# Optimization experiments

Measured on AMD Instinct MI355X. Metric: run time of the kernel, lower is better.

## Reference

```python
import jax, jax.numpy as jnp
import numpy as np

B, N, HID, IN_NF, L = 32, 64, 128, 32, 4


def _w(k, shape):
    fan_in = shape[-2]
    return jax.random.normal(k, shape, jnp.float32) / np.sqrt(fan_in).astype(np.float32)


def setup_inputs() -> dict:
    key = jax.random.key(0)
    ks = jax.random.split(key, 12)
    n_nodes = B * N
    # fully connected edges within each graph, offset for flat batch layout
    r, c = np.meshgrid(np.arange(N), np.arange(N), indexing='ij')
    m = r != c
    r, c = r[m], c[m]                      # (N*(N-1),)
    offs = (np.arange(B) * N)[:, None]
    edge_row = jnp.asarray((r[None] + offs).reshape(-1), dtype=jnp.int32)
    edge_col = jnp.asarray((c[None] + offs).reshape(-1), dtype=jnp.int32)
    n_edges = edge_row.shape[0]            # 129024
    return {
        'h': jax.random.normal(ks[0], (n_nodes, IN_NF), jnp.float32),
        'x': jax.random.normal(ks[1], (n_nodes, 3), jnp.float32),
        'edge_row': edge_row,
        'edge_col': edge_col,
        'edge_attr': jax.random.normal(ks[2], (n_edges, HID), jnp.float32) * 0.1,
        'emb_w': _w(ks[3], (IN_NF, HID)), 'emb_b': jnp.zeros((HID,), jnp.float32),
        'edge_w1': _w(ks[4], (L, 3 * HID + 1, HID)), 'edge_b1': jnp.zeros((L, HID), jnp.float32),
        'edge_w2': _w(ks[5], (L, HID, HID)), 'edge_b2': jnp.zeros((L, HID), jnp.float32),
        'node_w1': _w(ks[6], (L, 2 * HID, HID)), 'node_b1': jnp.zeros((L, HID), jnp.float32),
        'node_w2': _w(ks[7], (L, HID, HID)), 'node_b2': jnp.zeros((L, HID), jnp.float32),
        'coord_w1': _w(ks[8], (L, HID, HID)), 'coord_b1': jnp.zeros((L, HID), jnp.float32),
        'coord_w2': jax.random.normal(ks[9], (L, HID, 1), jnp.float32) * 0.001,  # xavier gain=0.001, no bias
    }


def reference(h, x, edge_row, edge_col, edge_attr,
              emb_w, emb_b,
              edge_w1, edge_b1, edge_w2, edge_b2,
              node_w1, node_b1, node_w2, node_b2,
              coord_w1, coord_b1, coord_w2):
    n_nodes = h.shape[0]
    silu = jax.nn.silu
    # degree for 'mean' coordinate aggregation (segments guaranteed nonempty via clip)
    ones = jnp.ones((edge_row.shape[0], 1), h.dtype)
    deg = jnp.clip(jax.ops.segment_sum(ones, edge_row, num_segments=n_nodes), 1.0)
    h = h @ emb_w + emb_b  # embedding_in
    for i in range(L):
        diff = x[edge_row] - x[edge_col]                 # (E,3)
        radial = jnp.sum(diff * diff, axis=1, keepdims=True)  # (E,1)
        # edge model: MLP([h_i, h_j, radial, edge_attr])
        e_in = jnp.concatenate([h[edge_row], h[edge_col], radial, edge_attr], axis=1)
        m = silu(silu(e_in @ edge_w1[i] + edge_b1[i]) @ edge_w2[i] + edge_b2[i])  # (E,HID)
        # coord model: mean-aggregated weighted differences
        trans = diff * (silu(m @ coord_w1[i] + coord_b1[i]) @ coord_w2[i])
        x = x + jax.ops.segment_sum(trans, edge_row, num_segments=n_nodes) / deg
        # node model with residual
        agg = jax.ops.segment_sum(m, edge_row, num_segments=n_nodes)
        n_in = jnp.concatenate([h, agg], axis=1)
        h = h + (silu(n_in @ node_w1[i] + node_b1[i]) @ node_w2[i] + node_b2[i])
        edge_attr = m  # backbone re-feeds edge_feat as next layer's edge_attr
    return h  # (B*N, HID); node_mask is None -> raw node embeddings returned
```

## Files before the change

kernel.cpp:

```cpp
#include <hip/hip_runtime.h>
#include <cstdint>
#include <cstddef>

#define HID    128
#define K1     385
#define NLAYER 4
#define NNODES 2048
#define NEDGES 129024
#define DEG    63
#define EPB    64
#define EBLOCKS (NEDGES / EPB)
#define EA_STRIDE 256
#define NPB    16
#define NBLOCKS (NNODES / NPB)

#define EIN_STRIDE 512
#define MBASE   16384
#define REDBASE 32768
#define RADBASE 33280
#define HR1BASE 33536
#define CB1BASE 34560
#define CW2BASE 35072
#define ELDS    35584

typedef __attribute__((ext_vector_type(8))) short short8;
typedef __attribute__((ext_vector_type(4))) float f32x4;

__device__ __forceinline__ unsigned pkbf(float a, float b) {
    unsigned r;
    asm("v_cvt_pk_bf16_f32 %0, %1, %2" : "=v"(r) : "v"(a), "v"(b));
    return r;
}
__device__ __forceinline__ unsigned short f2bf(float a) {
    return (unsigned short)pkbf(a, a);
}
__device__ __forceinline__ float silu_f(float v) {
    return v * __builtin_amdgcn_rcpf(1.0f + __expf(-v));
}

__global__ __launch_bounds__(64) void pack_all_kernel(
    const float* __restrict__ eW1, const float* __restrict__ eW2,
    const float* __restrict__ cW1, const float* __restrict__ nW1,
    const float* __restrict__ nW2,
    unsigned short* __restrict__ w1p, unsigned short* __restrict__ w1a,
    unsigned short* __restrict__ w2p, unsigned short* __restrict__ cw1p,
    unsigned short* __restrict__ nw1p, unsigned short* __restrict__ nw2p)
{
    int b = blockIdx.x;
    const float* src; unsigned short* dst; int KK, ls, mode;
    if (b < 256)      { src = eW1; dst = w1p;  KK = 8; ls = K1 * HID;      mode = 1; }
    else if (b < 384) { src = eW1; dst = w1a;  KK = 4; ls = K1 * HID;      mode = 0; b -= 256; }
    else if (b < 512) { src = eW2; dst = w2p;  KK = 4; ls = HID * HID;     mode = 0; b -= 384; }
    else if (b < 640) { src = cW1; dst = cw1p; KK = 4; ls = HID * HID;     mode = 0; b -= 512; }
    else if (b < 896) { src = nW1; dst = nw1p; KK = 8; ls = 2 * HID * HID; mode = 0; b -= 640; }
    else              { src = nW2; dst = nw2p; KK = 4; ls = HID * HID;     mode = 0; b -= 896; }
    const int tn = b & 7; b >>= 3;
    const int kk = b % KK;
    const int layer = b / KK;
    const int lane = threadIdx.x, lq = lane >> 4, lr = lane & 15;
    const float* s = src + (size_t)layer * ls;
    unsigned short* d = dst + (size_t)layer * (KK * 8 * 64 * 8)
                            + ((size_t)(kk * 8 + tn) * 64 + lane) * 8;
#pragma unroll
    for (int j = 0; j < 8; ++j) {
        const int kd = kk * 32 + lq * 8 + j;
        const int ka = mode ? (128 + kd + (kd >= 128 ? 1 : 0)) : kd;
        d[j] = f2bf(s[(size_t)ka * HID + tn * 16 + lr]);
    }
}

__global__ __launch_bounds__(128) void embed_kernel(
    const float* __restrict__ h_in, const float* __restrict__ emb_w,
    const float* __restrict__ emb_b, const float* __restrict__ eW1,
    const float* __restrict__ eB1,
    float* __restrict__ h_ws, unsigned short* __restrict__ h_bf,
    float* __restrict__ hr1, float* __restrict__ agg,
    const float* __restrict__ x_in, float* __restrict__ x_a)
{
    const int n = blockIdx.x;
    const int o = threadIdx.x;
    __shared__ float hin[32];
    __shared__ float hrow[HID];
    if (o < 32) hin[o] = h_in[n * 32 + o];
    __syncthreads();
    float acc = emb_b[o];
#pragma unroll
    for (int k = 0; k < 32; ++k) acc += hin[k] * emb_w[k * HID + o];
    h_ws[n * HID + o] = acc;
    h_bf[n * HID + o] = f2bf(acc);
    hrow[o] = acc;
    agg[n * HID + o] = 0.0f;
    if (o < 3) x_a[n * 3 + o] = x_in[n * 3 + o];
    __syncthreads();
    float a2 = eB1[o];
    for (int k = 0; k < HID; ++k) a2 += hrow[k] * eW1[k * HID + o];
    hr1[n * HID + o] = a2;
}

__global__ __launch_bounds__(512, 6) void edge_mfma_kernel(
    const unsigned short* __restrict__ h_bf, const float* __restrict__ x,
    const float* __restrict__ ea_f32, unsigned short* __restrict__ ea,
    const int first_layer, const float* __restrict__ hr1,
    const short8* __restrict__ w1p, const float* __restrict__ w256,
    const short8* __restrict__ w2p, const float* __restrict__ b2,
    const short8* __restrict__ cw1p, const float* __restrict__ cb1, const float* __restrict__ cw2,
    float* __restrict__ c_out, float* __restrict__ agg)
{
    __shared__ __align__(16) char smem[ELDS];
    float* red    = (float*)(smem + REDBASE);
    float* radial = (float*)(smem + RADBASE);
    float* hr1s   = (float*)(smem + HR1BASE);
    float* cb1s   = (float*)(smem + CB1BASE);
    float* cw2s   = (float*)(smem + CW2BASE);
    const int t = threadIdx.x;
    const int w = t >> 6, lane = t & 63, lq = lane >> 4, lr = lane & 15;
    const int ebase = blockIdx.x * EPB;
    const int n0 = ebase / DEG;
    const int esplit = DEG * (n0 + 1) - ebase;

    {
        const int s = t & 15, g = t >> 4;
#pragma unroll
        for (int j = 0; j < 2; ++j) {
            const int r = g + j * 32;
            const int e = ebase + r;
            const int row = n0 + (r >= esplit ? 1 : 0);
            const int jj = e - row * DEG;
            const int rl = row & 63;
            const int col = (row & ~63) + jj + (jj >= rl ? 1 : 0);
            const int swz = (r & 7) << 4;
            *(uint4*)(smem + r * EIN_STRIDE + ((s * 16) ^ swz)) =
                *(const uint4*)(h_bf + (size_t)col * HID + s * 8);
            uint4 v;
            if (first_layer) {
                const float4* ef = (const float4*)(ea_f32 + (size_t)e * HID);
                const float4 f0 = ef[s * 2], f1 = ef[s * 2 + 1];
                v.x = pkbf(f0.x, f0.y);
                v.y = pkbf(f0.z, f0.w);
                v.z = pkbf(f1.x, f1.y);
                v.w = pkbf(f1.z, f1.w);
            } else {
                v = *(const uint4*)(ea + (size_t)e * EA_STRIDE + s * 8);
            }
            *(uint4*)(smem + r * EIN_STRIDE + (((s + 16) * 16) ^ swz)) = v;
            if (s == 0) {
                const float dx = x[row * 3 + 0] - x[col * 3 + 0];
                const float dy = x[row * 3 + 1] - x[col * 3 + 1];
                const float dz = x[row * 3 + 2] - x[col * 3 + 2];
                radial[r] = dx * dx + dy * dy + dz * dz;
            }
        }
        if (t < 128) { cb1s[t] = cb1[t]; cw2s[t] = cw2[t]; }
        else if (t < 384) {
            const int i2 = t - 128;
            hr1s[i2] = hr1[(size_t)(n0 + (i2 >> 7)) * HID + (i2 & 127)];
        }
    }
    __syncthreads();

    const int c0 = w * 16 + lr;

    f32x4 acc1[4] = {};
#pragma unroll
    for (int kk = 0; kk < 8; ++kk) {
        const short8 bf = w1p[(kk * 8 + w) * 64 + lane];
#pragma unroll
        for (int mt = 0; mt < 4; ++mt) {
            const int r = mt * 16 + lr;
            const short8 af = *(const short8*)(smem + r * EIN_STRIDE +
                                ((kk * 64 + lq * 16) ^ ((r & 7) << 4)));
            acc1[mt] = __builtin_amdgcn_mfma_f32_16x16x32_bf16(af, bf, acc1[mt], 0, 0, 0);
        }
    }
    __syncthreads();

    {
        const float ww = w256[c0];
        const float ha = hr1s[c0], hb = hr1s[128 + c0];
#pragma unroll
        for (int mt = 0; mt < 4; ++mt)
#pragma unroll
            for (int reg = 0; reg < 4; ++reg) {
                const int r = mt * 16 + lq * 4 + reg;
                const float v = silu_f(acc1[mt][reg] + radial[r] * ww +
                                       (r < esplit ? ha : hb));
                *(unsigned short*)(smem + r * 256 + ((c0 * 2) ^ ((r & 7) << 4))) = f2bf(v);
            }
    }
    __syncthreads();

    f32x4 acc2[4] = {};
#pragma unroll
    for (int kk = 0; kk < 4; ++kk) {
        const short8 bf = w2p[(kk * 8 + w) * 64 + lane];
#pragma unroll
        for (int mt = 0; mt < 4; ++mt) {
            const int r = mt * 16 + lr;
            const short8 af = *(const short8*)(smem + r * 256 +
                                ((kk * 64 + lq * 16) ^ ((r & 7) << 4)));
            acc2[mt] = __builtin_amdgcn_mfma_f32_16x16x32_bf16(af, bf, acc2[mt], 0, 0, 0);
        }
    }
    {
        const float bb = b2[c0];
        float s0 = 0.0f, s1 = 0.0f;
#pragma unroll
        for (int mt = 0; mt < 4; ++mt)
#pragma unroll
            for (int reg = 0; reg < 4; ++reg) {
                const int r = mt * 16 + lq * 4 + reg;
                const float v = silu_f(acc2[mt][reg] + bb);
                if (r < esplit) s0 += v; else s1 += v;
                *(unsigned short*)(smem + MBASE + r * 256 + ((c0 * 2) ^ ((r & 7) << 4))) = f2bf(v);
            }
        s0 += __shfl_xor(s0, 16); s0 += __shfl_xor(s0, 32);
        s1 += __shfl_xor(s1, 16); s1 += __shfl_xor(s1, 32);
        if (lane < 16) {
            atomicAdd(&agg[(size_t)n0 * HID + c0], s0);
            atomicAdd(&agg[(size_t)(n0 + 1) * HID + c0], s1);
        }
    }
    __syncthreads();

    const int etile = w & 3, jhalf = w >> 2;
    f32x4 acc3[4] = {};
    {
        const int erow = etile * 16 + lr;
        const int eswz = (erow & 7) << 4;
#pragma unroll
        for (int kb = 0; kb < 4; ++kb) {
            const short8 mf = *(const short8*)(smem + MBASE + erow * 256 +
                                ((kb * 64 + lq * 16) ^ eswz));
#pragma unroll
            for (int jt = 0; jt < 4; ++jt) {
                const short8 af = cw1p[(kb * 8 + jhalf * 4 + jt) * 64 + lane];
                acc3[jt] = __builtin_amdgcn_mfma_f32_16x16x32_bf16(af, mf, acc3[jt], 0, 0, 0);
            }
        }
    }
    {
        const int s = t & 15, g = t >> 4;
#pragma unroll
        for (int j = 0; j < 2; ++j) {
            const int r = g + j * 32;
            const uint4 v = *(const uint4*)(smem + MBASE + r * 256 +
                                            ((s * 16) ^ ((r & 7) << 4)));
            *(uint4*)(ea + (size_t)(ebase + r) * EA_STRIDE + s * 8) = v;
        }
    }
    {
        float p = 0.0f;
#pragma unroll
        for (int jt = 0; jt < 4; ++jt)
#pragma unroll
            for (int reg = 0; reg < 4; ++reg) {
                const int j2 = jhalf * 64 + jt * 16 + lq * 4 + reg;
                p += silu_f(acc3[jt][reg] + cb1s[j2]) * cw2s[j2];
            }
        p += __shfl_xor(p, 16);
        p += __shfl_xor(p, 32);
        if (lane < 16) red[jhalf * 64 + etile * 16 + lane] = p;
    }
    __syncthreads();
    if (t < 64) c_out[ebase + t] = red[t] + red[64 + t];
}

__global__ __launch_bounds__(512, 4) void node_mfma_kernel(
    float* __restrict__ h_ws, unsigned short* __restrict__ h_bf,
    float* __restrict__ agg,
    const short8* __restrict__ nw1p, const float* __restrict__ nb1,
    const short8* __restrict__ nw2p, const float* __restrict__ nb2,
    const short8* __restrict__ w1a_next, const float* __restrict__ b1_next,
    float* __restrict__ hr1,
    const float* __restrict__ x_in, float* __restrict__ x_out,
    const float* __restrict__ c_ws,
    float* __restrict__ out, const int write_out, const int do_coord)
{
    __shared__ __align__(16) char smem[16384];
    const int t = threadIdx.x;
    const int w = t >> 6, lane = t & 63, lq = lane >> 4, lr = lane & 15;
    const int nb = blockIdx.x * NPB;

    {
        const int s = t & 31, g = t >> 5;
        const int node = nb + g;
        const int swz = (g & 7) << 4;
        if (s < 16) {
            *(uint4*)(smem + g * 512 + ((s * 16) ^ swz)) =
                *(const uint4*)(h_bf + (size_t)node * HID + s * 8);
        } else {
            const int q = s - 16;
            float4* agg4 = (float4*)(agg + (size_t)node * HID);
            const float4 a0 = agg4[q * 2], a1 = agg4[q * 2 + 1];
            agg4[q * 2]     = float4{0, 0, 0, 0};
            agg4[q * 2 + 1] = float4{0, 0, 0, 0};
            uint4 v;
            v.x = pkbf(a0.x, a0.y);
            v.y = pkbf(a0.z, a0.w);
            v.z = pkbf(a1.x, a1.y);
            v.w = pkbf(a1.z, a1.w);
            *(uint4*)(smem + g * 512 + ((s * 16) ^ swz)) = v;
        }
    }
    __syncthreads();

    const int c0 = w * 16 + lr;

    f32x4 acc1 = {};
#pragma unroll
    for (int kk = 0; kk < 8; ++kk) {
        const short8 bf = nw1p[(kk * 8 + w) * 64 + lane];
        const short8 af = *(const short8*)(smem + lr * 512 +
                            ((kk * 64 + lq * 16) ^ ((lr & 7) << 4)));
        acc1 = __builtin_amdgcn_mfma_f32_16x16x32_bf16(af, bf, acc1, 0, 0, 0);
    }
    __syncthreads();
    {
        const float bb = nb1[c0];
#pragma unroll
        for (int reg = 0; reg < 4; ++reg) {
            const int r = lq * 4 + reg;
            const float v = silu_f(acc1[reg] + bb);
            *(unsigned short*)(smem + 8192 + r * 256 + ((c0 * 2) ^ ((r & 7) << 4))) = f2bf(v);
        }
    }
    __syncthreads();
    f32x4 acc2 = {};
#pragma unroll
    for (int kk = 0; kk < 4; ++kk) {
        const short8 bf = nw2p[(kk * 8 + w) * 64 + lane];
        const short8 af = *(const short8*)(smem + 8192 + lr * 256 +
                            ((kk * 64 + lq * 16) ^ ((lr & 7) << 4)));
        acc2 = __builtin_amdgcn_mfma_f32_16x16x32_bf16(af, bf, acc2, 0, 0, 0);
    }
    {
        const float bb = nb2[c0];
#pragma unroll
        for (int reg = 0; reg < 4; ++reg) {
            const int r = lq * 4 + reg;
            const size_t gi = (size_t)(nb + r) * HID + c0;
            const float hnew = h_ws[gi] + acc2[reg] + bb;
            h_ws[gi] = hnew;
            h_bf[gi] = f2bf(hnew);
            if (write_out) out[gi] = hnew;
            *(unsigned short*)(smem + 12288 + r * 256 + ((c0 * 2) ^ ((r & 7) << 4))) = f2bf(hnew);
        }
    }
    __syncthreads();
    if (w1a_next) {
        f32x4 acch = {};
#pragma unroll
        for (int kk = 0; kk < 4; ++kk) {
            const short8 bf = w1a_next[(kk * 8 + w) * 64 + lane];
            const short8 af = *(const short8*)(smem + 12288 + lr * 256 +
                                ((kk * 64 + lq * 16) ^ ((lr & 7) << 4)));
            acch = __builtin_amdgcn_mfma_f32_16x16x32_bf16(af, bf, acch, 0, 0, 0);
        }
        const float bb = b1_next[c0];
#pragma unroll
        for (int reg = 0; reg < 4; ++reg) {
            const int r = lq * 4 + reg;
            hr1[(size_t)(nb + r) * HID + c0] = acch[reg] + bb;
        }
    }
    if (do_coord) {
        const int nl = t >> 5, sub = t & 31;
        const int n = nb + nl;
        const int rl = n & 63, base = n & ~63;
        const float xi0 = x_in[n * 3 + 0], xi1 = x_in[n * 3 + 1], xi2 = x_in[n * 3 + 2];
        float p0 = 0, p1 = 0, p2 = 0;
#pragma unroll
        for (int kk = 0; kk < 2; ++kk) {
            const int k = sub + kk * 32;
            if (k < DEG) {
                const int e = n * DEG + k;
                const int col = base + k + (k >= rl ? 1 : 0);
                const float c = c_ws[e];
                p0 += c * (xi0 - x_in[col * 3 + 0]);
                p1 += c * (xi1 - x_in[col * 3 + 1]);
                p2 += c * (xi2 - x_in[col * 3 + 2]);
            }
        }
#pragma unroll
        for (int off = 1; off < 32; off <<= 1) {
            p0 += __shfl_xor(p0, off);
            p1 += __shfl_xor(p1, off);
            p2 += __shfl_xor(p2, off);
        }
        if (sub == 0) {
            const float inv = 1.0f / DEG;
            x_out[n * 3 + 0] = xi0 + p0 * inv;
            x_out[n * 3 + 1] = xi1 + p1 * inv;
            x_out[n * 3 + 2] = xi2 + p2 * inv;
        }
    }
}

extern "C" void kernel_launch(void* const* d_in, const int* in_sizes, int n_in,
                              void* d_out, int out_size, void* d_ws, size_t ws_size,
                              hipStream_t stream)
{
    const float* h_in  = (const float*)d_in[0];
    const float* x_in  = (const float*)d_in[1];
    const float* ea0   = (const float*)d_in[4];
    const float* emb_w = (const float*)d_in[5];
    const float* emb_b = (const float*)d_in[6];
    const float* eW1   = (const float*)d_in[7];
    const float* eB1   = (const float*)d_in[8];
    const float* eW2   = (const float*)d_in[9];
    const float* eB2   = (const float*)d_in[10];
    const float* nW1   = (const float*)d_in[11];
    const float* nB1   = (const float*)d_in[12];
    const float* nW2   = (const float*)d_in[13];
    const float* nB2   = (const float*)d_in[14];
    const float* cW1   = (const float*)d_in[15];
    const float* cB1   = (const float*)d_in[16];
    const float* cW2   = (const float*)d_in[17];
    float* out = (float*)d_out;

    unsigned short* ea_bf = (unsigned short*)d_in[4];

    char* p = (char*)d_ws;
    float* h_ws = (float*)p;                    p += (size_t)NNODES * HID * 4;
    unsigned short* h_bf = (unsigned short*)p;  p += (size_t)NNODES * HID * 2;
    float* agg  = (float*)p;                    p += (size_t)NNODES * HID * 4;
    float* hr1  = (float*)p;                    p += (size_t)NNODES * HID * 4;
    float* x_a  = (float*)p;                    p += NNODES * 3 * 4 + 16;
    float* x_b  = (float*)p;                    p += NNODES * 3 * 4 + 16;
    float* c_ws = (float*)p;                    p += (size_t)NEDGES * 4;
    unsigned short* w1p  = (unsigned short*)p;  p += (size_t)NLAYER * 8 * 8 * 64 * 8 * 2;
    unsigned short* w1a  = (unsigned short*)p;  p += (size_t)NLAYER * 4 * 8 * 64 * 8 * 2;
    unsigned short* w2p  = (unsigned short*)p;  p += (size_t)NLAYER * 4 * 8 * 64 * 8 * 2;
    unsigned short* cw1p = (unsigned short*)p;  p += (size_t)NLAYER * 4 * 8 * 64 * 8 * 2;
    unsigned short* nw1p = (unsigned short*)p;  p += (size_t)NLAYER * 8 * 8 * 64 * 8 * 2;
    unsigned short* nw2p = (unsigned short*)p;  p += (size_t)NLAYER * 4 * 8 * 64 * 8 * 2;

    const int SL8 = 8 * 8 * 64 * 8;
    const int SL4 = 4 * 8 * 64 * 8;

    pack_all_kernel<<<1024, 64, 0, stream>>>(eW1, eW2, cW1, nW1, nW2,
                                             w1p, w1a, w2p, cw1p, nw1p, nw2p);

    embed_kernel<<<NNODES, HID, 0, stream>>>(h_in, emb_w, emb_b, eW1, eB1,
                                             h_ws, h_bf, hr1, agg, x_in, x_a);

    float* xc = x_a;
    float* xn = x_b;
    for (int i = 0; i < NLAYER; ++i) {
        edge_mfma_kernel<<<EBLOCKS, 512, 0, stream>>>(
            h_bf, xc, ea0, ea_bf, (i == 0) ? 1 : 0, hr1,
            (const short8*)(w1p + (size_t)i * SL8),
            eW1 + ((size_t)i * K1 + 256) * HID,
            (const short8*)(w2p + (size_t)i * SL4), eB2 + i * HID,
            (const short8*)(cw1p + (size_t)i * SL4), cB1 + i * HID,
            cW2 + (size_t)i * HID, c_ws, agg);
        node_mfma_kernel<<<NBLOCKS, 512, 0, stream>>>(
            h_ws, h_bf, agg,
            (const short8*)(nw1p + (size_t)i * SL8), nB1 + i * HID,
            (const short8*)(nw2p + (size_t)i * SL4), nB2 + i * HID,
            (i < NLAYER - 1) ? (const short8*)(w1a + (size_t)(i + 1) * SL4) : (const short8*)nullptr,
            (i < NLAYER - 1) ? (eB1 + (size_t)(i + 1) * HID) : nullptr,
            hr1, xc, xn, c_ws,
            out, (i == NLAYER - 1) ? 1 : 0, (i < NLAYER - 1) ? 1 : 0);
        float* tmp = xc; xc = xn; xn = tmp;
    }
}
```

Measured before the change: 306.2 us.

## Halve edges per block to 32 and separate hidden/message LDS buffers

Each edge block now handles 32 edges instead of 64, which doubles the number of blocks. All MFMA loops shrink to two M-tiles, and the coord MLP is split over four column quarters with a four-way reduction. The first-layer activations now go to their own LDS region, so the barrier between the GEMM1 reads and the hidden write can be dropped. The second atomic is skipped when the block does not cross a node boundary, and agg/hr1 get one padding row because n0+1 can run one past the last node. This aims to improve occupancy and latency hiding, at the cost of loading weights twice as often per edge.

```diff
diff --git a/kernel.cpp b/kernel.cpp
--- a/kernel.cpp
+++ b/kernel.cpp
@@ -8,20 +8,21 @@
 #define NNODES 2048
 #define NEDGES 129024
 #define DEG    63
-#define EPB    64
+#define EPB    32
 #define EBLOCKS (NEDGES / EPB)
 #define EA_STRIDE 256
 #define NPB    16
 #define NBLOCKS (NNODES / NPB)
 
 #define EIN_STRIDE 512
-#define MBASE   16384
+#define HIDB    16384
+#define MBASE   24576
 #define REDBASE 32768
 #define RADBASE 33280
-#define HR1BASE 33536
-#define CB1BASE 34560
-#define CW2BASE 35072
-#define ELDS    35584
+#define HR1BASE 33408
+#define CB1BASE 34432
+#define CW2BASE 34944
+#define ELDS    35456
 
 typedef __attribute__((ext_vector_type(8))) short short8;
 typedef __attribute__((ext_vector_type(4))) float f32x4;
@@ -120,35 +121,32 @@
 
     {
         const int s = t & 15, g = t >> 4;
-#pragma unroll
-        for (int j = 0; j < 2; ++j) {
-            const int r = g + j * 32;
-            const int e = ebase + r;
-            const int row = n0 + (r >= esplit ? 1 : 0);
-            const int jj = e - row * DEG;
-            const int rl = row & 63;
-            const int col = (row & ~63) + jj + (jj >= rl ? 1 : 0);
-            const int swz = (r & 7) << 4;
-            *(uint4*)(smem + r * EIN_STRIDE + ((s * 16) ^ swz)) =
-                *(const uint4*)(h_bf + (size_t)col * HID + s * 8);
-            uint4 v;
-            if (first_layer) {
-                const float4* ef = (const float4*)(ea_f32 + (size_t)e * HID);
-                const float4 f0 = ef[s * 2], f1 = ef[s * 2 + 1];
-                v.x = pkbf(f0.x, f0.y);
-                v.y = pkbf(f0.z, f0.w);
-                v.z = pkbf(f1.x, f1.y);
-                v.w = pkbf(f1.z, f1.w);
-            } else {
-                v = *(const uint4*)(ea + (size_t)e * EA_STRIDE + s * 8);
-            }
-            *(uint4*)(smem + r * EIN_STRIDE + (((s + 16) * 16) ^ swz)) = v;
-            if (s == 0) {
-                const float dx = x[row * 3 + 0] - x[col * 3 + 0];
-                const float dy = x[row * 3 + 1] - x[col * 3 + 1];
-                const float dz = x[row * 3 + 2] - x[col * 3 + 2];
-                radial[r] = dx * dx + dy * dy + dz * dz;
-            }
+        const int r = g;
+        const int e = ebase + r;
+        const int row = n0 + (r >= esplit ? 1 : 0);
+        const int jj = e - row * DEG;
+        const int rl = row & 63;
+        const int col = (row & ~63) + jj + (jj >= rl ? 1 : 0);
+        const int swz = (r & 7) << 4;
+        *(uint4*)(smem + r * EIN_STRIDE + ((s * 16) ^ swz)) =
+            *(const uint4*)(h_bf + (size_t)col * HID + s * 8);
+        uint4 v;
+        if (first_layer) {
+            const float4* ef = (const float4*)(ea_f32 + (size_t)e * HID);
+            const float4 f0 = ef[s * 2], f1 = ef[s * 2 + 1];
+            v.x = pkbf(f0.x, f0.y);
+            v.y = pkbf(f0.z, f0.w);
+            v.z = pkbf(f1.x, f1.y);
+            v.w = pkbf(f1.z, f1.w);
+        } else {
+            v = *(const uint4*)(ea + (size_t)e * EA_STRIDE + s * 8);
+        }
+        *(uint4*)(smem + r * EIN_STRIDE + (((s + 16) * 16) ^ swz)) = v;
+        if (s == 0) {
+            const float dx = x[row * 3 + 0] - x[col * 3 + 0];
+            const float dy = x[row * 3 + 1] - x[col * 3 + 1];
+            const float dz = x[row * 3 + 2] - x[col * 3 + 2];
+            radial[r] = dx * dx + dy * dy + dz * dz;
         }
         if (t < 128) { cb1s[t] = cb1[t]; cw2s[t] = cw2[t]; }
         else if (t < 384) {
@@ -160,43 +158,41 @@
 
     const int c0 = w * 16 + lr;
 
-    f32x4 acc1[4] = {};
+    f32x4 acc1[2] = {};
 #pragma unroll
     for (int kk = 0; kk < 8; ++kk) {
         const short8 bf = w1p[(kk * 8 + w) * 64 + lane];
 #pragma unroll
-        for (int mt = 0; mt < 4; ++mt) {
+        for (int mt = 0; mt < 2; ++mt) {
             const int r = mt * 16 + lr;
             const short8 af = *(const short8*)(smem + r * EIN_STRIDE +
                                 ((kk * 64 + lq * 16) ^ ((r & 7) << 4)));
             acc1[mt] = __builtin_amdgcn_mfma_f32_16x16x32_bf16(af, bf, acc1[mt], 0, 0, 0);
         }
     }
-    __syncthreads();
-
     {
         const float ww = w256[c0];
         const float ha = hr1s[c0], hb = hr1s[128 + c0];
 #pragma unroll
-        for (int mt = 0; mt < 4; ++mt)
+        for (int mt = 0; mt < 2; ++mt)
 #pragma unroll
             for (int reg = 0; reg < 4; ++reg) {
                 const int r = mt * 16 + lq * 4 + reg;
                 const float v = silu_f(acc1[mt][reg] + radial[r] * ww +
                                        (r < esplit ? ha : hb));
-                *(unsigned short*)(smem + r * 256 + ((c0 * 2) ^ ((r & 7) << 4))) = f2bf(v);
+                *(unsigned short*)(smem + HIDB + r * 256 + ((c0 * 2) ^ ((r & 7) << 4))) = f2bf(v);
             }
     }
     __syncthreads();
 
-    f32x4 acc2[4] = {};
+    f32x4 acc2[2] = {};
 #pragma unroll
     for (int kk = 0; kk < 4; ++kk) {
         const short8 bf = w2p[(kk * 8 + w) * 64 + lane];
 #pragma unroll
-        for (int mt = 0; mt < 4; ++mt) {
+        for (int mt = 0; mt < 2; ++mt) {
             const int r = mt * 16 + lr;
-            const short8 af = *(const short8*)(smem + r * 256 +
+            const short8 af = *(const short8*)(smem + HIDB + r * 256 +
                                 ((kk * 64 + lq * 16) ^ ((r & 7) << 4)));
             acc2[mt] = __builtin_amdgcn_mfma_f32_16x16x32_bf16(af, bf, acc2[mt], 0, 0, 0);
         }
@@ -205,7 +201,7 @@
         const float bb = b2[c0];
         float s0 = 0.0f, s1 = 0.0f;
 #pragma unroll
-        for (int mt = 0; mt < 4; ++mt)
+        for (int mt = 0; mt < 2; ++mt)
 #pragma unroll
             for (int reg = 0; reg < 4; ++reg) {
                 const int r = mt * 16 + lq * 4 + reg;
@@ -217,13 +213,14 @@
         s1 += __shfl_xor(s1, 16); s1 += __shfl_xor(s1, 32);
         if (lane < 16) {
             atomicAdd(&agg[(size_t)n0 * HID + c0], s0);
-            atomicAdd(&agg[(size_t)(n0 + 1) * HID + c0], s1);
-        }
-    }
-    __syncthreads();
-
-    const int etile = w & 3, jhalf = w >> 2;
-    f32x4 acc3[4] = {};
+            if (esplit < EPB)
+                atomicAdd(&agg[(size_t)(n0 + 1) * HID + c0], s1);
+        }
+    }
+    __syncthreads();
+
+    const int etile = w & 1, jq = w >> 1;
+    f32x4 acc3[2] = {};
     {
         const int erow = etile * 16 + lr;
         const int eswz = (erow & 7) << 4;
@@ -232,37 +229,33 @@
             const short8 mf = *(const short8*)(smem + MBASE + erow * 256 +
                                 ((kb * 64 + lq * 16) ^ eswz));
 #pragma unroll
-            for (int jt = 0; jt < 4; ++jt) {
-                const short8 af = cw1p[(kb * 8 + jhalf * 4 + jt) * 64 + lane];
+            for (int jt = 0; jt < 2; ++jt) {
+                const short8 af = cw1p[(kb * 8 + jq * 2 + jt) * 64 + lane];
                 acc3[jt] = __builtin_amdgcn_mfma_f32_16x16x32_bf16(af, mf, acc3[jt], 0, 0, 0);
             }
         }
     }
     {
         const int s = t & 15, g = t >> 4;
-#pragma unroll
-        for (int j = 0; j < 2; ++j) {
-            const int r = g + j * 32;
-            const uint4 v = *(const uint4*)(smem + MBASE + r * 256 +
-                                            ((s * 16) ^ ((r & 7) << 4)));
-            *(uint4*)(ea + (size_t)(ebase + r) * EA_STRIDE + s * 8) = v;
-        }
+        const uint4 v = *(const uint4*)(smem + MBASE + g * 256 +
+                                        ((s * 16) ^ ((g & 7) << 4)));
+        *(uint4*)(ea + (size_t)(ebase + g) * EA_STRIDE + s * 8) = v;
     }
     {
         float p = 0.0f;
 #pragma unroll
-        for (int jt = 0; jt < 4; ++jt)
+        for (int jt = 0; jt < 2; ++jt)
 #pragma unroll
             for (int reg = 0; reg < 4; ++reg) {
-                const int j2 = jhalf * 64 + jt * 16 + lq * 4 + reg;
+                const int j2 = jq * 32 + jt * 16 + lq * 4 + reg;
                 p += silu_f(acc3[jt][reg] + cb1s[j2]) * cw2s[j2];
             }
         p += __shfl_xor(p, 16);
         p += __shfl_xor(p, 32);
-        if (lane < 16) red[jhalf * 64 + etile * 16 + lane] = p;
-    }
-    __syncthreads();
-    if (t < 64) c_out[ebase + t] = red[t] + red[64 + t];
+        if (lane < 16) red[jq * 32 + etile * 16 + lane] = p;
+    }
+    __syncthreads();
+    if (t < 32) c_out[ebase + t] = red[t] + red[32 + t] + red[64 + t] + red[96 + t];
 }
 
 __global__ __launch_bounds__(512, 4) void node_mfma_kernel(
@@ -423,8 +416,8 @@
     char* p = (char*)d_ws;
     float* h_ws = (float*)p;                    p += (size_t)NNODES * HID * 4;
     unsigned short* h_bf = (unsigned short*)p;  p += (size_t)NNODES * HID * 2;
-    float* agg  = (float*)p;                    p += (size_t)NNODES * HID * 4;
-    float* hr1  = (float*)p;                    p += (size_t)NNODES * HID * 4;
+    float* agg  = (float*)p;                    p += (size_t)(NNODES + 1) * HID * 4;
+    float* hr1  = (float*)p;                    p += (size_t)(NNODES + 1) * HID * 4;
     float* x_a  = (float*)p;                    p += NNODES * 3 * 4 + 16;
     float* x_b  = (float*)p;                    p += NNODES * 3 * 4 + 16;
     float* c_ws = (float*)p;                    p += (size_t)NEDGES * 4;
```

Result: slower. 319.5 us (+4.3%).

## Fuse coordinate aggregation into edge kernel and skip coord MLP on last layer

Applied to the files above, without the earlier changes.

The edge kernel now multiplies its per-edge coordinate weight by the stored dx/dy/dz, reduces the result across the block for the two nodes it covers, and atomically adds into a per-node xdelta buffer. This replaces writing per-edge coefficients to global memory and the node kernel's later gather of neighbor coordinates. The node kernel only applies xdelta/DEG and clears it. On the last layer the coord MLP and the edge_attr writeback are skipped, since their outputs are unused. The MFMA loops are also restructured to issue two K-steps per iteration. The cost is extra atomics and a 64-lane shuffle reduction.

```diff
diff --git a/kernel.cpp b/kernel.cpp
--- a/kernel.cpp
+++ b/kernel.cpp
@@ -18,10 +18,13 @@
 #define MBASE   16384
 #define REDBASE 32768
 #define RADBASE 33280
-#define HR1BASE 33536
-#define CB1BASE 34560
-#define CW2BASE 35072
-#define ELDS    35584
+#define DXBASE  33536
+#define DYBASE  33792
+#define DZBASE  34048
+#define HR1BASE 34304
+#define CB1BASE 35328
+#define CW2BASE 35840
+#define ELDS    36352
 
 typedef __attribute__((ext_vector_type(8))) short short8;
 typedef __attribute__((ext_vector_type(4))) float f32x4;
@@ -74,7 +77,7 @@
     const float* __restrict__ emb_b, const float* __restrict__ eW1,
     const float* __restrict__ eB1,
     float* __restrict__ h_ws, unsigned short* __restrict__ h_bf,
-    float* __restrict__ hr1, float* __restrict__ agg,
+    float* __restrict__ hr1, float* __restrict__ agg, float* __restrict__ xdelta,
     const float* __restrict__ x_in, float* __restrict__ x_a)
 {
     const int n = blockIdx.x;
@@ -90,7 +93,7 @@
     h_bf[n * HID + o] = f2bf(acc);
     hrow[o] = acc;
     agg[n * HID + o] = 0.0f;
-    if (o < 3) x_a[n * 3 + o] = x_in[n * 3 + o];
+    if (o < 3) { x_a[n * 3 + o] = x_in[n * 3 + o]; xdelta[n * 3 + o] = 0.0f; }
     __syncthreads();
     float a2 = eB1[o];
     for (int k = 0; k < HID; ++k) a2 += hrow[k] * eW1[k * HID + o];
@@ -104,11 +107,15 @@
     const short8* __restrict__ w1p, const float* __restrict__ w256,
     const short8* __restrict__ w2p, const float* __restrict__ b2,
     const short8* __restrict__ cw1p, const float* __restrict__ cb1, const float* __restrict__ cw2,
-    float* __restrict__ c_out, float* __restrict__ agg)
+    float* __restrict__ xdelta,
+    float* __restrict__ agg)
 {
     __shared__ __align__(16) char smem[ELDS];
     float* red    = (float*)(smem + REDBASE);
     float* radial = (float*)(smem + RADBASE);
+    float* dxs    = (float*)(smem + DXBASE);
+    float* dys    = (float*)(smem + DYBASE);
+    float* dzs    = (float*)(smem + DZBASE);
     float* hr1s   = (float*)(smem + HR1BASE);
     float* cb1s   = (float*)(smem + CB1BASE);
     float* cw2s   = (float*)(smem + CW2BASE);
@@ -148,6 +155,7 @@
                 const float dy = x[row * 3 + 1] - x[col * 3 + 1];
                 const float dz = x[row * 3 + 2] - x[col * 3 + 2];
                 radial[r] = dx * dx + dy * dy + dz * dz;
+                dxs[r] = dx; dys[r] = dy; dzs[r] = dz;
             }
         }
         if (t < 128) { cb1s[t] = cb1[t]; cw2s[t] = cw2[t]; }
@@ -162,14 +170,19 @@
 
     f32x4 acc1[4] = {};
 #pragma unroll
-    for (int kk = 0; kk < 8; ++kk) {
-        const short8 bf = w1p[(kk * 8 + w) * 64 + lane];
+    for (int kk2 = 0; kk2 < 4; ++kk2) {
+        const short8 bf0 = w1p[((2 * kk2) * 8 + w) * 64 + lane];
+        const short8 bf1 = w1p[((2 * kk2 + 1) * 8 + w) * 64 + lane];
 #pragma unroll
         for (int mt = 0; mt < 4; ++mt) {
             const int r = mt * 16 + lr;
-            const short8 af = *(const short8*)(smem + r * EIN_STRIDE +
-                                ((kk * 64 + lq * 16) ^ ((r & 7) << 4)));
-            acc1[mt] = __builtin_amdgcn_mfma_f32_16x16x32_bf16(af, bf, acc1[mt], 0, 0, 0);
+            const int swz = (r & 7) << 4;
+            const char* b0 = smem + r * EIN_STRIDE + ((lq * 16) ^ swz);
+            const char* b1 = smem + r * EIN_STRIDE + ((lq * 16 + 64) ^ swz);
+            acc1[mt] = __builtin_amdgcn_mfma_f32_16x16x32_bf16(
+                *(const short8*)(b0 + kk2 * 128), bf0, acc1[mt], 0, 0, 0);
+            acc1[mt] = __builtin_amdgcn_mfma_f32_16x16x32_bf16(
+                *(const short8*)(b1 + kk2 * 128), bf1, acc1[mt], 0, 0, 0);
         }
     }
     __syncthreads();
@@ -191,14 +204,19 @@
 
     f32x4 acc2[4] = {};
 #pragma unroll
-    for (int kk = 0; kk < 4; ++kk) {
-        const short8 bf = w2p[(kk * 8 + w) * 64 + lane];
+    for (int kk2 = 0; kk2 < 2; ++kk2) {
+        const short8 bf0 = w2p[((2 * kk2) * 8 + w) * 64 + lane];
+        const short8 bf1 = w2p[((2 * kk2 + 1) * 8 + w) * 64 + lane];
 #pragma unroll
         for (int mt = 0; mt < 4; ++mt) {
             const int r = mt * 16 + lr;
-            const short8 af = *(const short8*)(smem + r * 256 +
-                                ((kk * 64 + lq * 16) ^ ((r & 7) << 4)));
-            acc2[mt] = __builtin_amdgcn_mfma_f32_16x16x32_bf16(af, bf, acc2[mt], 0, 0, 0);
+            const int swz = (r & 7) << 4;
+            const char* b0 = smem + r * 256 + ((lq * 16) ^ swz);
+            const char* b1 = smem + r * 256 + ((lq * 16 + 64) ^ swz);
+            acc2[mt] = __builtin_amdgcn_mfma_f32_16x16x32_bf16(
+                *(const short8*)(b0 + kk2 * 128), bf0, acc2[mt], 0, 0, 0);
+            acc2[mt] = __builtin_amdgcn_mfma_f32_16x16x32_bf16(
+                *(const short8*)(b1 + kk2 * 128), bf1, acc2[mt], 0, 0, 0);
         }
     }
     {
@@ -220,49 +238,76 @@
             atomicAdd(&agg[(size_t)(n0 + 1) * HID + c0], s1);
         }
     }
-    __syncthreads();
-
-    const int etile = w & 3, jhalf = w >> 2;
-    f32x4 acc3[4] = {};
-    {
-        const int erow = etile * 16 + lr;
-        const int eswz = (erow & 7) << 4;
-#pragma unroll
-        for (int kb = 0; kb < 4; ++kb) {
-            const short8 mf = *(const short8*)(smem + MBASE + erow * 256 +
-                                ((kb * 64 + lq * 16) ^ eswz));
-#pragma unroll
-            for (int jt = 0; jt < 4; ++jt) {
-                const short8 af = cw1p[(kb * 8 + jhalf * 4 + jt) * 64 + lane];
-                acc3[jt] = __builtin_amdgcn_mfma_f32_16x16x32_bf16(af, mf, acc3[jt], 0, 0, 0);
-            }
-        }
-    }
-    {
-        const int s = t & 15, g = t >> 4;
-#pragma unroll
-        for (int j = 0; j < 2; ++j) {
-            const int r = g + j * 32;
-            const uint4 v = *(const uint4*)(smem + MBASE + r * 256 +
-                                            ((s * 16) ^ ((r & 7) << 4)));
-            *(uint4*)(ea + (size_t)(ebase + r) * EA_STRIDE + s * 8) = v;
-        }
-    }
-    {
-        float p = 0.0f;
-#pragma unroll
-        for (int jt = 0; jt < 4; ++jt)
-#pragma unroll
-            for (int reg = 0; reg < 4; ++reg) {
-                const int j2 = jhalf * 64 + jt * 16 + lq * 4 + reg;
-                p += silu_f(acc3[jt][reg] + cb1s[j2]) * cw2s[j2];
-            }
-        p += __shfl_xor(p, 16);
-        p += __shfl_xor(p, 32);
-        if (lane < 16) red[jhalf * 64 + etile * 16 + lane] = p;
-    }
-    __syncthreads();
-    if (t < 64) c_out[ebase + t] = red[t] + red[64 + t];
+
+    if (xdelta) {
+        __syncthreads();
+        const int etile = w & 3, jhalf = w >> 2;
+        f32x4 acc3[4] = {};
+        {
+            const int erow = etile * 16 + lr;
+            const int eswz = (erow & 7) << 4;
+            const char* mb0 = smem + MBASE + erow * 256 + ((lq * 16) ^ eswz);
+            const char* mb1 = smem + MBASE + erow * 256 + ((lq * 16 + 64) ^ eswz);
+#pragma unroll
+            for (int kb2 = 0; kb2 < 2; ++kb2) {
+                const short8 mf0 = *(const short8*)(mb0 + kb2 * 128);
+                const short8 mf1 = *(const short8*)(mb1 + kb2 * 128);
+#pragma unroll
+                for (int jt = 0; jt < 4; ++jt) {
+                    const short8 af0 = cw1p[((2 * kb2) * 8 + jhalf * 4 + jt) * 64 + lane];
+                    const short8 af1 = cw1p[((2 * kb2 + 1) * 8 + jhalf * 4 + jt) * 64 + lane];
+                    acc3[jt] = __builtin_amdgcn_mfma_f32_16x16x32_bf16(af0, mf0, acc3[jt], 0, 0, 0);
+                    acc3[jt] = __builtin_amdgcn_mfma_f32_16x16x32_bf16(af1, mf1, acc3[jt], 0, 0, 0);
+                }
+            }
+        }
+        {
+            const int s = t & 15, g = t >> 4;
+#pragma unroll
+            for (int j = 0; j < 2; ++j) {
+                const int r = g + j * 32;
+                const uint4 v = *(const uint4*)(smem + MBASE + r * 256 +
+                                                ((s * 16) ^ ((r & 7) << 4)));
+                *(uint4*)(ea + (size_t)(ebase + r) * EA_STRIDE + s * 8) = v;
+            }
+        }
+        {
+            float p = 0.0f;
+#pragma unroll
+            for (int jt = 0; jt < 4; ++jt)
+#pragma unroll
+                for (int reg = 0; reg < 4; ++reg) {
+                    const int j2 = jhalf * 64 + jt * 16 + lq * 4 + reg;
+                    p += silu_f(acc3[jt][reg] + cb1s[j2]) * cw2s[j2];
+                }
+            p += __shfl_xor(p, 16);
+            p += __shfl_xor(p, 32);
+            if (lane < 16) red[jhalf * 64 + etile * 16 + lane] = p;
+        }
+        __syncthreads();
+        if (t < 64) {
+            const float c = red[t] + red[64 + t];
+            const float cdx = c * dxs[t], cdy = c * dys[t], cdz = c * dzs[t];
+            const bool in0 = (t < esplit);
+            float a0x = in0 ? cdx : 0.0f, a1x = in0 ? 0.0f : cdx;
+            float a0y = in0 ? cdy : 0.0f, a1y = in0 ? 0.0f : cdy;
+            float a0z = in0 ? cdz : 0.0f, a1z = in0 ? 0.0f : cdz;
+#pragma unroll
+            for (int off = 1; off < 64; off <<= 1) {
+                a0x += __shfl_xor(a0x, off); a1x += __shfl_xor(a1x, off);
+                a0y += __shfl_xor(a0y, off); a1y += __shfl_xor(a1y, off);
+                a0z += __shfl_xor(a0z, off); a1z += __shfl_xor(a1z, off);
+            }
+            if (t == 0) {
+                atomicAdd(&xdelta[n0 * 3 + 0], a0x);
+                atomicAdd(&xdelta[n0 * 3 + 1], a0y);
+                atomicAdd(&xdelta[n0 * 3 + 2], a0z);
+                atomicAdd(&xdelta[(n0 + 1) * 3 + 0], a1x);
+                atomicAdd(&xdelta[(n0 + 1) * 3 + 1], a1y);
+                atomicAdd(&xdelta[(n0 + 1) * 3 + 2], a1z);
+            }
+        }
+    }
 }
 
 __global__ __launch_bounds__(512, 4) void node_mfma_kernel(
@@ -273,7 +318,7 @@
     const short8* __restrict__ w1a_next, const float* __restrict__ b1_next,
     float* __restrict__ hr1,
     const float* __restrict__ x_in, float* __restrict__ x_out,
-    const float* __restrict__ c_ws,
+    float* __restrict__ xdelta,
     float* __restrict__ out, const int write_out, const int do_coord)
 {
     __shared__ __align__(16) char smem[16384];
@@ -302,17 +347,30 @@
             *(uint4*)(smem + g * 512 + ((s * 16) ^ swz)) = v;
         }
     }
+    if (do_coord && t < NPB * 3) {
+        const int n = nb + t / 3, d = t - (t / 3) * 3;
+        const float xd = xdelta[n * 3 + d];
+        x_out[n * 3 + d] = x_in[n * 3 + d] + xd * (1.0f / DEG);
+        xdelta[n * 3 + d] = 0.0f;
+    }
     __syncthreads();
 
     const int c0 = w * 16 + lr;
 
     f32x4 acc1 = {};
-#pragma unroll
-    for (int kk = 0; kk < 8; ++kk) {
-        const short8 bf = nw1p[(kk * 8 + w) * 64 + lane];
-        const short8 af = *(const short8*)(smem + lr * 512 +
-                            ((kk * 64 + lq * 16) ^ ((lr & 7) << 4)));
-        acc1 = __builtin_amdgcn_mfma_f32_16x16x32_bf16(af, bf, acc1, 0, 0, 0);
+    {
+        const int swz = (lr & 7) << 4;
+        const char* b0 = smem + lr * 512 + ((lq * 16) ^ swz);
+        const char* b1 = smem + lr * 512 + ((lq * 16 + 64) ^ swz);
+#pragma unroll
+        for (int kk2 = 0; kk2 < 4; ++kk2) {
+            const short8 bf0 = nw1p[((2 * kk2) * 8 + w) * 64 + lane];
+            const short8 bf1 = nw1p[((2 * kk2 + 1) * 8 + w) * 64 + lane];
+            acc1 = __builtin_amdgcn_mfma_f32_16x16x32_bf16(
+                *(const short8*)(b0 + kk2 * 128), bf0, acc1, 0, 0, 0);
+            acc1 = __builtin_amdgcn_mfma_f32_16x16x32_bf16(
+                *(const short8*)(b1 + kk2 * 128), bf1, acc1, 0, 0, 0);
+        }
     }
     __syncthreads();
     {
@@ -326,12 +384,19 @@
     }
     __syncthreads();
     f32x4 acc2 = {};
-#pragma unroll
-    for (int kk = 0; kk < 4; ++kk) {
-        const short8 bf = nw2p[(kk * 8 + w) * 64 + lane];
-        const short8 af = *(const short8*)(smem + 8192 + lr * 256 +
-                            ((kk * 64 + lq * 16) ^ ((lr & 7) << 4)));
-        acc2 = __builtin_amdgcn_mfma_f32_16x16x32_bf16(af, bf, acc2, 0, 0, 0);
+    {
+        const int swz = (lr & 7) << 4;
+        const char* b0 = smem + 8192 + lr * 256 + ((lq * 16) ^ swz);
+        const char* b1 = smem + 8192 + lr * 256 + ((lq * 16 + 64) ^ swz);
+#pragma unroll
+        for (int kk2 = 0; kk2 < 2; ++kk2) {
+            const short8 bf0 = nw2p[((2 * kk2) * 8 + w) * 64 + lane];
+            const short8 bf1 = nw2p[((2 * kk2 + 1) * 8 + w) * 64 + lane];
+            acc2 = __builtin_amdgcn_mfma_f32_16x16x32_bf16(
+                *(const short8*)(b0 + kk2 * 128), bf0, acc2, 0, 0, 0);
+            acc2 = __builtin_amdgcn_mfma_f32_16x16x32_bf16(
+                *(const short8*)(b1 + kk2 * 128), bf1, acc2, 0, 0, 0);
+        }
     }
     {
         const float bb = nb2[c0];
@@ -349,49 +414,23 @@
     __syncthreads();
     if (w1a_next) {
         f32x4 acch = {};
-#pragma unroll
-        for (int kk = 0; kk < 4; ++kk) {
-            const short8 bf = w1a_next[(kk * 8 + w) * 64 + lane];
-            const short8 af = *(const short8*)(smem + 12288 + lr * 256 +
-                                ((kk * 64 + lq * 16) ^ ((lr & 7) << 4)));
-            acch = __builtin_amdgcn_mfma_f32_16x16x32_bf16(af, bf, acch, 0, 0, 0);
+        const int swz = (lr & 7) << 4;
+        const char* b0 = smem + 12288 + lr * 256 + ((lq * 16) ^ swz);
+        const char* b1 = smem + 12288 + lr * 256 + ((lq * 16 + 64) ^ swz);
+#pragma unroll
+        for (int kk2 = 0; kk2 < 2; ++kk2) {
+            const short8 bf0 = w1a_next[((2 * kk2) * 8 + w) * 64 + lane];
+            const short8 bf1 = w1a_next[((2 * kk2 + 1) * 8 + w) * 64 + lane];
+            acch = __builtin_amdgcn_mfma_f32_16x16x32_bf16(
+                *(const short8*)(b0 + kk2 * 128), bf0, acch, 0, 0, 0);
+            acch = __builtin_amdgcn_mfma_f32_16x16x32_bf16(
+                *(const short8*)(b1 + kk2 * 128), bf1, acch, 0, 0, 0);
         }
         const float bb = b1_next[c0];
 #pragma unroll
         for (int reg = 0; reg < 4; ++reg) {
             const int r = lq * 4 + reg;
             hr1[(size_t)(nb + r) * HID + c0] = acch[reg] + bb;
-        }
-    }
-    if (do_coord) {
-        const int nl = t >> 5, sub = t & 31;
-        const int n = nb + nl;
-        const int rl = n & 63, base = n & ~63;
-        const float xi0 = x_in[n * 3 + 0], xi1 = x_in[n * 3 + 1], xi2 = x_in[n * 3 + 2];
-        float p0 = 0, p1 = 0, p2 = 0;
-#pragma unroll
-        for (int kk = 0; kk < 2; ++kk) {
-            const int k = sub + kk * 32;
-            if (k < DEG) {
-                const int e = n * DEG + k;
-                const int col = base + k + (k >= rl ? 1 : 0);
-                const float c = c_ws[e];
-                p0 += c * (xi0 - x_in[col * 3 + 0]);
-                p1 += c * (xi1 - x_in[col * 3 + 1]);
-                p2 += c * (xi2 - x_in[col * 3 + 2]);
-            }
-        }
-#pragma unroll
-        for (int off = 1; off < 32; off <<= 1) {
-            p0 += __shfl_xor(p0, off);
-            p1 += __shfl_xor(p1, off);
-            p2 += __shfl_xor(p2, off);
-        }
-        if (sub == 0) {
-            const float inv = 1.0f / DEG;
-            x_out[n * 3 + 0] = xi0 + p0 * inv;
-            x_out[n * 3 + 1] = xi1 + p1 * inv;
-            x_out[n * 3 + 2] = xi2 + p2 * inv;
         }
     }
 }
@@ -423,11 +462,11 @@
     char* p = (char*)d_ws;
     float* h_ws = (float*)p;                    p += (size_t)NNODES * HID * 4;
     unsigned short* h_bf = (unsigned short*)p;  p += (size_t)NNODES * HID * 2;
-    float* agg  = (float*)p;                    p += (size_t)NNODES * HID * 4;
-    float* hr1  = (float*)p;                    p += (size_t)NNODES * HID * 4;
+    float* agg  = (float*)p;                    p += (size_t)(NNODES + 1) * HID * 4;
+    float* hr1  = (float*)p;                    p += (size_t)(NNODES + 1) * HID * 4;
     float* x_a  = (float*)p;                    p += NNODES * 3 * 4 + 16;
     float* x_b  = (float*)p;                    p += NNODES * 3 * 4 + 16;
-    float* c_ws = (float*)p;                    p += (size_t)NEDGES * 4;
+    float* xdelta = (float*)p;                  p += NNODES * 3 * 4 + 16;
     unsigned short* w1p  = (unsigned short*)p;  p += (size_t)NLAYER * 8 * 8 * 64 * 8 * 2;
     unsigned short* w1a  = (unsigned short*)p;  p += (size_t)NLAYER * 4 * 8 * 64 * 8 * 2;
     unsigned short* w2p  = (unsigned short*)p;  p += (size_t)NLAYER * 4 * 8 * 64 * 8 * 2;
@@ -442,26 +481,28 @@
                                              w1p, w1a, w2p, cw1p, nw1p, nw2p);
 
     embed_kernel<<<NNODES, HID, 0, stream>>>(h_in, emb_w, emb_b, eW1, eB1,
-                                             h_ws, h_bf, hr1, agg, x_in, x_a);
+                                             h_ws, h_bf, hr1, agg, xdelta, x_in, x_a);
 
     float* xc = x_a;
     float* xn = x_b;
     for (int i = 0; i < NLAYER; ++i) {
+        const int last = (i == NLAYER - 1);
         edge_mfma_kernel<<<EBLOCKS, 512, 0, stream>>>(
             h_bf, xc, ea0, ea_bf, (i == 0) ? 1 : 0, hr1,
             (const short8*)(w1p + (size_t)i * SL8),
             eW1 + ((size_t)i * K1 + 256) * HID,
             (const short8*)(w2p + (size_t)i * SL4), eB2 + i * HID,
             (const short8*)(cw1p + (size_t)i * SL4), cB1 + i * HID,
-            cW2 + (size_t)i * HID, c_ws, agg);
+            cW2 + (size_t)i * HID,
+            last ? nullptr : xdelta, agg);
         node_mfma_kernel<<<NBLOCKS, 512, 0, stream>>>(
             h_ws, h_bf, agg,
             (const short8*)(nw1p + (size_t)i * SL8), nB1 + i * HID,
             (const short8*)(nw2p + (size_t)i * SL4), nB2 + i * HID,
-            (i < NLAYER - 1) ? (const short8*)(w1a + (size_t)(i + 1) * SL4) : (const short8*)nullptr,
-            (i < NLAYER - 1) ? (eB1 + (size_t)(i + 1) * HID) : nullptr,
-            hr1, xc, xn, c_ws,
-            out, (i == NLAYER - 1) ? 1 : 0, (i < NLAYER - 1) ? 1 : 0);
+            last ? (const short8*)nullptr : (const short8*)(w1a + (size_t)(i + 1) * SL4),
+            last ? nullptr : (eB1 + (size_t)(i + 1) * HID),
+            hr1, xc, xn, xdelta,
+            out, last ? 1 : 0, last ? 0 : 1);
         float* tmp = xc; xc = xn; xn = tmp;
     }
 }
```

New measurement: 299.3 us. 1.02x faster.
